# Kernel optimization log

Hardware: AMD Instinct MI355X
Metric: run time of the kernel (lower is better)

Reference implementation:

```python
import jax, jax.numpy as jnp
import numpy as np

NUM_CAPSULES = 10
NUM_ROUTES = 4096  # 64 * 8 * 8
IN_CHANNELS = 8
OUT_CHANNELS = 16
BATCH = 128
NUM_ITERATIONS = 3


def squash(s):
    # s: [B, C, O]; squash along capsule-vector dim O (torch dim=-2 of [B,1,C,O,1])
    squared_norm = jnp.sum(s * s, axis=-1, keepdims=True)
    return squared_norm * s / ((1.0 + squared_norm) * jnp.sqrt(squared_norm))


def setup_inputs() -> dict:
    key = jax.random.key(0)
    k1, k2, k3 = jax.random.split(key, 3)
    x = jax.random.normal(k1, (BATCH, NUM_ROUTES, IN_CHANNELS), dtype=jnp.float32)
    W = 0.01 * jax.random.normal(k2, (NUM_ROUTES, NUM_CAPSULES, OUT_CHANNELS, IN_CHANNELS), dtype=jnp.float32)
    bias = 0.01 * jax.random.normal(k3, (NUM_CAPSULES, OUT_CHANNELS), dtype=jnp.float32)
    return {"x": x, "W": W, "bias": bias}


def reference(x, W, bias):
    # u_hat[b,r,c,o] = sum_i W[r,c,o,i] * x[b,r,i]
    u_hat = jnp.einsum('rcoi,bri->brco', W, x)  # [B,R,C,O]
    B = x.shape[0]
    b_ij = jnp.zeros((B, NUM_ROUTES, NUM_CAPSULES), dtype=u_hat.dtype)
    v = None
    for it in range(NUM_ITERATIONS):
        c_ij = jax.nn.softmax(b_ij, axis=2)                    # softmax over capsules
        s = jnp.einsum('brc,brco->bco', c_ij, u_hat) + bias    # [B,C,O]
        v = squash(s)                                          # [B,C,O]
        if it < NUM_ITERATIONS - 1:
            a = jnp.einsum('brco,bco->brc', u_hat, v)          # agreement
            b_ij = b_ij + a
    # torch returns v_j.squeeze(1): [B, C, O, 1]
    return v[..., None]
```

## Files before the change

kernel.cpp:

```cpp
#include <hip/hip_runtime.h>
#include <math.h>

constexpr int B  = 128;
constexpr int R  = 4096;
constexpr int IC = 8;
constexpr int C  = 10;
constexpr int O  = 16;
constexpr int CO = C * O;

constexpr int RCH    = 16;
constexpr int NCHUNK = R / RCH;
constexpr int NWCONV = (R * C * O * IC) / 1024;
constexpr int NXPOSE = (R / 16) * (B / 16);

using f16x8 = __attribute__((ext_vector_type(8))) _Float16;
using f16x4 = __attribute__((ext_vector_type(4))) _Float16;
using f32x4 = __attribute__((ext_vector_type(4))) float;

template<int CTRL>
__device__ __forceinline__ float dpp_add(float v) {
    return v + __int_as_float(__builtin_amdgcn_update_dpp(
        0, __float_as_int(v), CTRL, 0xF, 0xF, true));
}
__device__ __forceinline__ float rowsum16(float v) {
    v = dpp_add<0x121>(v); v = dpp_add<0x122>(v);
    v = dpp_add<0x124>(v); v = dpp_add<0x128>(v);
    return v;
}

__device__ __forceinline__ float sum_kb(float p) {
    p += __int_as_float(__builtin_amdgcn_ds_swizzle(__float_as_int(p), 0x401F));
    p += __shfl_xor(p, 32, 64);
    return p;
}

__global__ __launch_bounds__(256)
void convert_kernel(const float* __restrict__ x, const float* __restrict__ W,
                    _Float16* __restrict__ W16, _Float16* __restrict__ xT16)
{
    const int bid = blockIdx.x;
    const int tid = threadIdx.x;
    if (bid < NWCONV) {
        const size_t i = ((size_t)bid * 256 + tid) * 4;
        float4 v = *reinterpret_cast<const float4*>(W + i);
        f16x4 h = {(_Float16)v.x, (_Float16)v.y, (_Float16)v.z, (_Float16)v.w};
        *reinterpret_cast<f16x4*>(W16 + i) = h;
    } else {
        __shared__ float tile[16][16][IC + 1];
        const int v  = bid - NWCONV;
        const int r0 = (v & 255) * 16;
        const int b0 = (v >> 8) * 16;
        {
            const int rj = tid & 15, bi = tid >> 4;
            const float* src = x + ((size_t)(b0 + bi) * R + (r0 + rj)) * IC;
            float4 a0 = *reinterpret_cast<const float4*>(src);
            float4 a1 = *reinterpret_cast<const float4*>(src + 4);
            float* t = tile[bi][rj];
            t[0]=a0.x; t[1]=a0.y; t[2]=a0.z; t[3]=a0.w;
            t[4]=a1.x; t[5]=a1.y; t[6]=a1.z; t[7]=a1.w;
        }
        __syncthreads();
        {
            const int bi = tid & 15, rj = tid >> 4;
            const float* t = tile[bi][rj];
            f16x8 h;
            #pragma unroll
            for (int i = 0; i < IC; ++i) h[i] = (_Float16)t[i];
            *reinterpret_cast<f16x8*>(xT16 + ((size_t)(r0 + rj) * B + (b0 + bi)) * IC) = h;
        }
    }
}

__global__ __launch_bounds__(256, 4)
void pass0_gemm(const _Float16* __restrict__ W16, const _Float16* __restrict__ xT16,
                _Float16* __restrict__ s_part)
{
    const int tid = threadIdx.x;
    const int wv  = tid >> 6;
    const int l   = tid & 63;
    const int ln  = l & 15;
    const int kb  = l >> 4;

    const int g     = blockIdx.x;
    const int xcd   = g & 7;
    const int t     = g >> 3;
    const int bhalf = t & 1;
    const int cid   = t >> 1;
    const int chunk = xcd * 32 + cid;
    const int b     = bhalf * 64 + wv * 16 + ln;
    const int r0    = chunk * RCH;

    f32x4 sacc[C];
    #pragma unroll
    for (int c = 0; c < C; ++c) sacc[c] = (f32x4){0.f, 0.f, 0.f, 0.f};

    const _Float16* xptr = xT16 + ((size_t)(r0 + kb) * B + b) * IC;
    const _Float16* wptr = W16 + ((size_t)(r0 + kb) * C * O + ln) * IC;

    #pragma unroll 2
    for (int rp = 0; rp < RCH / 4; ++rp) {
        const f16x8 bf = *reinterpret_cast<const f16x8*>(xptr);
        xptr += (size_t)4 * B * IC;
        #pragma unroll
        for (int c = 0; c < C; ++c) {
            f16x8 af = *reinterpret_cast<const f16x8*>(wptr + (size_t)c * (O * IC));
            sacc[c] = __builtin_amdgcn_mfma_f32_16x16x32_f16(af, bf, sacc[c], 0, 0, 0);
        }
        wptr += (size_t)4 * C * O * IC;
    }

    _Float16* sp = s_part + ((size_t)chunk * B + b) * CO + kb * 4;
    #pragma unroll
    for (int c = 0; c < C; ++c) {
        f16x4 h = {(_Float16)(sacc[c][0] * 0.1f), (_Float16)(sacc[c][1] * 0.1f),
                   (_Float16)(sacc[c][2] * 0.1f), (_Float16)(sacc[c][3] * 0.1f)};
        *reinterpret_cast<f16x4*>(sp + c * O) = h;
    }
}

template<int IT>
__global__ __launch_bounds__(256, 2)
void pass_mfma(const _Float16* __restrict__ W16, const _Float16* __restrict__ xT16,
               const float* __restrict__ vsum, _Float16* __restrict__ s_part)
{
    __shared__ _Float16 wlds[RCH * C * O * IC];
    __shared__ _Float16 xlds[RCH * 64 * IC];

    const int tid = threadIdx.x;
    const int wv  = tid >> 6;
    const int l   = tid & 63;
    const int ln  = l & 15;
    const int kb  = l >> 4;

    const int g     = blockIdx.x;
    const int xcd   = g & 7;
    const int t     = g >> 3;
    const int bhalf = t & 1;
    const int cid   = t >> 1;
    const int chunk = xcd * 32 + cid;
    const int b     = bhalf * 64 + wv * 16 + ln;
    const int r0    = chunk * RCH;

    {
        const _Float16* wsrc = W16 + (size_t)r0 * (C * O * IC);
        #pragma unroll
        for (int k = 0; k < 10; ++k) {
            const int idx = (k * 256 + tid) * 8;
            *reinterpret_cast<f16x8*>(&wlds[idx]) =
                *reinterpret_cast<const f16x8*>(wsrc + idx);
        }
    }
    {
        const int rr = tid >> 6, lx = tid & 63;
        #pragma unroll
        for (int k = 0; k < 4; ++k) {
            const int r = rr + k * 4;
            *reinterpret_cast<f16x8*>(&xlds[(r * 64 + lx) * IC]) =
                *reinterpret_cast<const f16x8*>(
                    xT16 + ((size_t)(r0 + r) * B + bhalf * 64 + lx) * IC);
        }
    }

    float vreg[C][4];
    #pragma unroll
    for (int c = 0; c < C; ++c)
        *reinterpret_cast<float4*>(vreg[c]) =
            *reinterpret_cast<const float4*>(vsum + (size_t)b * CO + c * O + kb * 4);

    f32x4 sacc[C];
    #pragma unroll
    for (int c = 0; c < C; ++c) sacc[c] = (f32x4){0.f, 0.f, 0.f, 0.f};

    __syncthreads();

    const int bloc = wv * 16 + ln;

    #pragma unroll 2
    for (int rr = 0; rr < RCH; ++rr) {
        f16x8 bf;
        #pragma unroll
        for (int j = 0; j < 8; ++j) bf[j] = (_Float16)0.f;
        if (kb == 0)
            bf = *reinterpret_cast<const f16x8*>(&xlds[(rr * 64 + bloc) * IC]);

        f32x4 uh[C];
        #pragma unroll
        for (int c = 0; c < C; ++c) {
            f16x8 af = *reinterpret_cast<const f16x8*>(
                &wlds[((rr * C + c) * O + ln) * IC]);
            uh[c] = __builtin_amdgcn_mfma_f32_16x16x32_f16(
                        af, bf, (f32x4){0.f, 0.f, 0.f, 0.f}, 0, 0, 0);
        }

        float a[C];
        #pragma unroll
        for (int c = 0; c < C; ++c) {
            float p = uh[c][0] * vreg[c][0];
            p = fmaf(uh[c][1], vreg[c][1], p);
            p = fmaf(uh[c][2], vreg[c][2], p);
            p = fmaf(uh[c][3], vreg[c][3], p);
            a[c] = sum_kb(p);
        }
        float sum = 0.f;
        #pragma unroll
        for (int c = 0; c < C; ++c) { a[c] = __expf(a[c]); sum += a[c]; }
        const float inv = __builtin_amdgcn_rcpf(sum);
        #pragma unroll
        for (int c = 0; c < C; ++c) {
            const float wgt = a[c] * inv;
            #pragma unroll
            for (int j = 0; j < 4; ++j)
                sacc[c][j] = fmaf(wgt, uh[c][j], sacc[c][j]);
        }
    }

    _Float16* sp = s_part + ((size_t)chunk * B + b) * CO + kb * 4;
    #pragma unroll
    for (int c = 0; c < C; ++c) {
        f16x4 h = {(_Float16)sacc[c][0], (_Float16)sacc[c][1],
                   (_Float16)sacc[c][2], (_Float16)sacc[c][3]};
        *reinterpret_cast<f16x4*>(sp + c * O) = h;
    }
}

__global__ __launch_bounds__(256)
void reduce_squash(const _Float16* __restrict__ s_part, const float* __restrict__ bias,
                   const float* __restrict__ vin_sum,
                   float* __restrict__ v_out, float* __restrict__ vsum_out)
{
    const int b = blockIdx.x;
    const int c = blockIdx.y;
    const int t = threadIdx.x;
    const int o = t & 15;
    const int q = t >> 4;

    float acc = 0.f;
    for (int k = 0; k < NCHUNK / 16; ++k) {
        const int blk = q * (NCHUNK / 16) + k;
        acc += (float)s_part[((size_t)blk * B + b) * CO + c * O + o];
    }
    __shared__ float red[16][O];
    red[q][o] = acc;
    __syncthreads();

    if (t < O) {
        float s = bias[c * O + o];
        #pragma unroll
        for (int k = 0; k < 16; ++k) s += red[k][o];
        float n = rowsum16(s * s);
        float v = s * sqrtf(n) / (1.f + n);
        const size_t idx = (size_t)b * CO + c * O + o;
        if (v_out)    v_out[idx] = v;
        if (vsum_out) vsum_out[idx] = (vin_sum ? vin_sum[idx] : 0.f) + v;
    }
}

extern "C" void kernel_launch(void* const* d_in, const int* in_sizes, int n_in,
                              void* d_out, int out_size, void* d_ws, size_t ws_size,
                              hipStream_t stream)
{
    const float* x    = (const float*)d_in[0];
    const float* W    = (const float*)d_in[1];
    const float* bias = (const float*)d_in[2];
    float* out = (float*)d_out;

    float* ws      = (float*)d_ws;
    float* vsumA   = ws;
    float* vsumB   = vsumA + (size_t)B * CO;
    _Float16* s_part = (_Float16*)(vsumB + (size_t)B * CO);
    _Float16* W16    = s_part + (size_t)NCHUNK * B * CO;
    _Float16* xT16   = W16 + (size_t)R * C * O * IC;

    convert_kernel<<<NWCONV + NXPOSE, 256, 0, stream>>>(x, W, W16, xT16);

    dim3 pg(NCHUNK * 2);
    dim3 rg(B, C);

    pass0_gemm<<<pg, 256, 0, stream>>>(W16, xT16, s_part);
    reduce_squash<<<rg, 256, 0, stream>>>(s_part, bias, nullptr, nullptr, vsumA);
    pass_mfma<1><<<pg, 256, 0, stream>>>(W16, xT16, vsumA, s_part);
    reduce_squash<<<rg, 256, 0, stream>>>(s_part, bias, vsumA, nullptr, vsumB);
    pass_mfma<2><<<pg, 256, 0, stream>>>(W16, xT16, vsumB, s_part);
    reduce_squash<<<rg, 256, 0, stream>>>(s_part, bias, nullptr, out, nullptr);
}
```

Baseline: 84.30 us.

## Fuse fp32-to-fp16 conversion and transpose into the first routing GEMM pass

Removes the separate conversion kernel and has the first pass read fp32 W and x directly, convert them to fp16 into LDS, and run the MFMA from LDS. The same blocks also write the fp16 W and transposed x copies to global memory for the later passes, with W written only by the bhalf==0 blocks. This saves one kernel launch and a global round trip of the converted data before pass 0. In exchange, each chunk's W is read twice in fp32 (once per batch half), and occupancy drops from 4 to 2 blocks because of the LDS use.

```diff
diff --git a/kernel.cpp b/kernel.cpp
--- a/kernel.cpp
+++ b/kernel.cpp
@@ -10,8 +10,6 @@
 
 constexpr int RCH    = 16;
 constexpr int NCHUNK = R / RCH;
-constexpr int NWCONV = (R * C * O * IC) / 1024;
-constexpr int NXPOSE = (R / 16) * (B / 16);
 
 using f16x8 = __attribute__((ext_vector_type(8))) _Float16;
 using f16x4 = __attribute__((ext_vector_type(4))) _Float16;
@@ -34,47 +32,102 @@
     return p;
 }
 
-__global__ __launch_bounds__(256)
-void convert_kernel(const float* __restrict__ x, const float* __restrict__ W,
-                    _Float16* __restrict__ W16, _Float16* __restrict__ xT16)
-{
-    const int bid = blockIdx.x;
+__global__ __launch_bounds__(256, 2)
+void pass0_fused(const float* __restrict__ x, const float* __restrict__ W,
+                 _Float16* __restrict__ W16, _Float16* __restrict__ xT16,
+                 _Float16* __restrict__ s_part)
+{
+    __shared__ _Float16 wlds[RCH * C * O * IC];
+    __shared__ _Float16 xlds[RCH * 64 * IC];
+
     const int tid = threadIdx.x;
-    if (bid < NWCONV) {
-        const size_t i = ((size_t)bid * 256 + tid) * 4;
-        float4 v = *reinterpret_cast<const float4*>(W + i);
-        f16x4 h = {(_Float16)v.x, (_Float16)v.y, (_Float16)v.z, (_Float16)v.w};
-        *reinterpret_cast<f16x4*>(W16 + i) = h;
-    } else {
-        __shared__ float tile[16][16][IC + 1];
-        const int v  = bid - NWCONV;
-        const int r0 = (v & 255) * 16;
-        const int b0 = (v >> 8) * 16;
-        {
-            const int rj = tid & 15, bi = tid >> 4;
-            const float* src = x + ((size_t)(b0 + bi) * R + (r0 + rj)) * IC;
-            float4 a0 = *reinterpret_cast<const float4*>(src);
-            float4 a1 = *reinterpret_cast<const float4*>(src + 4);
-            float* t = tile[bi][rj];
-            t[0]=a0.x; t[1]=a0.y; t[2]=a0.z; t[3]=a0.w;
-            t[4]=a1.x; t[5]=a1.y; t[6]=a1.z; t[7]=a1.w;
-        }
-        __syncthreads();
-        {
-            const int bi = tid & 15, rj = tid >> 4;
-            const float* t = tile[bi][rj];
-            f16x8 h;
-            #pragma unroll
-            for (int i = 0; i < IC; ++i) h[i] = (_Float16)t[i];
-            *reinterpret_cast<f16x8*>(xT16 + ((size_t)(r0 + rj) * B + (b0 + bi)) * IC) = h;
-        }
-    }
-}
-
-__global__ __launch_bounds__(256, 4)
-void pass0_gemm(const _Float16* __restrict__ W16, const _Float16* __restrict__ xT16,
-                _Float16* __restrict__ s_part)
-{
+    const int wv  = tid >> 6;
+    const int l   = tid & 63;
+    const int ln  = l & 15;
+    const int kb  = l >> 4;
+
+    const int g     = blockIdx.x;
+    const int xcd   = g & 7;
+    const int t     = g >> 3;
+    const int bhalf = t & 1;
+    const int cid   = t >> 1;
+    const int chunk = xcd * 32 + cid;
+    const int b     = bhalf * 64 + wv * 16 + ln;
+    const int b0    = bhalf * 64;
+    const int r0    = chunk * RCH;
+
+    {
+        const float* wsrc = W + (size_t)r0 * (C * O * IC);
+        _Float16*    wdst = W16 + (size_t)r0 * (C * O * IC);
+        #pragma unroll
+        for (int k = 0; k < 20; ++k) {
+            const int idx = (k * 256 + tid) * 4;
+            float4 v = *reinterpret_cast<const float4*>(wsrc + idx);
+            f16x4 h = {(_Float16)v.x, (_Float16)v.y, (_Float16)v.z, (_Float16)v.w};
+            *reinterpret_cast<f16x4*>(&wlds[idx]) = h;
+            if (bhalf == 0)
+                *reinterpret_cast<f16x4*>(wdst + idx) = h;
+        }
+    }
+    {
+        #pragma unroll
+        for (int k = 0; k < 8; ++k) {
+            const int w2 = k * 256 + tid;
+            const int bi = w2 >> 5, f4 = w2 & 31;
+            const int r = f4 >> 1, i4 = f4 & 1;
+            float4 v = *reinterpret_cast<const float4*>(
+                x + ((size_t)(b0 + bi) * R + r0 + r) * IC + i4 * 4);
+            f16x4 h = {(_Float16)v.x, (_Float16)v.y, (_Float16)v.z, (_Float16)v.w};
+            *reinterpret_cast<f16x4*>(&xlds[(r * 64 + bi) * IC + i4 * 4]) = h;
+        }
+    }
+    __syncthreads();
+    {
+        #pragma unroll
+        for (int k = 0; k < 4; ++k) {
+            const int w2 = k * 256 + tid;
+            const int r = w2 >> 6, v = w2 & 63;
+            *reinterpret_cast<f16x8*>(
+                xT16 + ((size_t)(r0 + r) * B + b0 + v) * IC) =
+                *reinterpret_cast<const f16x8*>(&xlds[(r * 64 + v) * IC]);
+        }
+    }
+
+    f32x4 sacc[C];
+    #pragma unroll
+    for (int c = 0; c < C; ++c) sacc[c] = (f32x4){0.f, 0.f, 0.f, 0.f};
+
+    const int bloc = wv * 16 + ln;
+
+    #pragma unroll 2
+    for (int rp = 0; rp < RCH / 4; ++rp) {
+        const int r = rp * 4 + kb;
+        const f16x8 bf = *reinterpret_cast<const f16x8*>(&xlds[(r * 64 + bloc) * IC]);
+        #pragma unroll
+        for (int c = 0; c < C; ++c) {
+            f16x8 af = *reinterpret_cast<const f16x8*>(
+                &wlds[((r * C + c) * O + ln) * IC]);
+            sacc[c] = __builtin_amdgcn_mfma_f32_16x16x32_f16(af, bf, sacc[c], 0, 0, 0);
+        }
+    }
+
+    _Float16* sp = s_part + ((size_t)chunk * B + b) * CO + kb * 4;
+    #pragma unroll
+    for (int c = 0; c < C; ++c) {
+        f16x4 h = {(_Float16)(sacc[c][0] * 0.1f), (_Float16)(sacc[c][1] * 0.1f),
+                   (_Float16)(sacc[c][2] * 0.1f), (_Float16)(sacc[c][3] * 0.1f)};
+        *reinterpret_cast<f16x4*>(sp + c * O) = h;
+    }
+}
+
+template<int IT>
+__global__ __launch_bounds__(256, 2)
+void pass_mfma(const _Float16* __restrict__ W16, const _Float16* __restrict__ xT16,
+               const float* __restrict__ vsum, _Float16* __restrict__ s_part)
+{
+    __shared__ _Float16 wlds[RCH * C * O * IC];
+    __shared__ _Float16 xlds[RCH * 64 * IC];
+
     const int tid = threadIdx.x;
     const int wv  = tid >> 6;
     const int l   = tid & 63;
@@ -90,57 +143,6 @@
     const int b     = bhalf * 64 + wv * 16 + ln;
     const int r0    = chunk * RCH;
 
-    f32x4 sacc[C];
-    #pragma unroll
-    for (int c = 0; c < C; ++c) sacc[c] = (f32x4){0.f, 0.f, 0.f, 0.f};
-
-    const _Float16* xptr = xT16 + ((size_t)(r0 + kb) * B + b) * IC;
-    const _Float16* wptr = W16 + ((size_t)(r0 + kb) * C * O + ln) * IC;
-
-    #pragma unroll 2
-    for (int rp = 0; rp < RCH / 4; ++rp) {
-        const f16x8 bf = *reinterpret_cast<const f16x8*>(xptr);
-        xptr += (size_t)4 * B * IC;
-        #pragma unroll
-        for (int c = 0; c < C; ++c) {
-            f16x8 af = *reinterpret_cast<const f16x8*>(wptr + (size_t)c * (O * IC));
-            sacc[c] = __builtin_amdgcn_mfma_f32_16x16x32_f16(af, bf, sacc[c], 0, 0, 0);
-        }
-        wptr += (size_t)4 * C * O * IC;
-    }
-
-    _Float16* sp = s_part + ((size_t)chunk * B + b) * CO + kb * 4;
-    #pragma unroll
-    for (int c = 0; c < C; ++c) {
-        f16x4 h = {(_Float16)(sacc[c][0] * 0.1f), (_Float16)(sacc[c][1] * 0.1f),
-                   (_Float16)(sacc[c][2] * 0.1f), (_Float16)(sacc[c][3] * 0.1f)};
-        *reinterpret_cast<f16x4*>(sp + c * O) = h;
-    }
-}
-
-template<int IT>
-__global__ __launch_bounds__(256, 2)
-void pass_mfma(const _Float16* __restrict__ W16, const _Float16* __restrict__ xT16,
-               const float* __restrict__ vsum, _Float16* __restrict__ s_part)
-{
-    __shared__ _Float16 wlds[RCH * C * O * IC];
-    __shared__ _Float16 xlds[RCH * 64 * IC];
-
-    const int tid = threadIdx.x;
-    const int wv  = tid >> 6;
-    const int l   = tid & 63;
-    const int ln  = l & 15;
-    const int kb  = l >> 4;
-
-    const int g     = blockIdx.x;
-    const int xcd   = g & 7;
-    const int t     = g >> 3;
-    const int bhalf = t & 1;
-    const int cid   = t >> 1;
-    const int chunk = xcd * 32 + cid;
-    const int b     = bhalf * 64 + wv * 16 + ln;
-    const int r0    = chunk * RCH;
-
     {
         const _Float16* wsrc = W16 + (size_t)r0 * (C * O * IC);
         #pragma unroll
@@ -271,12 +273,10 @@
     _Float16* W16    = s_part + (size_t)NCHUNK * B * CO;
     _Float16* xT16   = W16 + (size_t)R * C * O * IC;
 
-    convert_kernel<<<NWCONV + NXPOSE, 256, 0, stream>>>(x, W, W16, xT16);
-
     dim3 pg(NCHUNK * 2);
     dim3 rg(B, C);
 
-    pass0_gemm<<<pg, 256, 0, stream>>>(W16, xT16, s_part);
+    pass0_fused<<<pg, 256, 0, stream>>>(x, W, W16, xT16, s_part);
     reduce_squash<<<rg, 256, 0, stream>>>(s_part, bias, nullptr, nullptr, vsumA);
     pass_mfma<1><<<pg, 256, 0, stream>>>(W16, xT16, vsumA, s_part);
     reduce_squash<<<rg, 256, 0, stream>>>(s_part, bias, vsumA, nullptr, vsumB);
```

Measured after the change: 73.72 us, median of 2. 12.6% less time.
